# Kernel tuning notes

Hardware: AMD Instinct MI355X
Metric: run time of the kernel (lower is better)

Reference implementation:

```python
import jax, jax.numpy as jnp
import numpy as np

B, L, IN_DIM, D, H = 4, 1024, 256, 512, 8
DH = D // H
LARGE_NEG = -10000.0
LN_EPS = 1e-5


def _layernorm(x, g, b):
    mu = jnp.mean(x, axis=-1, keepdims=True)
    var = jnp.mean((x - mu) ** 2, axis=-1, keepdims=True)
    return (x - mu) * jax.lax.rsqrt(var + LN_EPS) * g + b


def setup_inputs() -> dict:
    key = jax.random.key(0)
    ks = jax.random.split(key, 16)
    s = 0.02
    return {
        "x": jax.random.normal(ks[0], (B, L, IN_DIM), jnp.float32),
        "attention_mask": jax.random.bernoulli(ks[1], 0.5, (B, L, L)),
        "adjacency_matrix": jax.random.uniform(ks[2], (B, L, L), jnp.float32),
        "W_fuse": jax.random.normal(ks[3], (D, IN_DIM), jnp.float32) * s,
        "b_fuse": jnp.zeros((D,), jnp.float32),
        "in_proj_w": jax.random.normal(ks[4], (3 * D, D), jnp.float32) * s,
        "in_proj_b": jnp.zeros((3 * D,), jnp.float32),
        "out_w": jax.random.normal(ks[5], (D, D), jnp.float32) * s,
        "out_b": jnp.zeros((D,), jnp.float32),
        "ln1_g": jnp.ones((D,), jnp.float32),
        "ln1_b": jnp.zeros((D,), jnp.float32),
        "ln2_g": jnp.ones((D,), jnp.float32),
        "ln2_b": jnp.zeros((D,), jnp.float32),
        "W1": jax.random.normal(ks[6], (4 * D, D), jnp.float32) * s,
        "b1": jnp.zeros((4 * D,), jnp.float32),
        "W2": jax.random.normal(ks[7], (D, 4 * D), jnp.float32) * s,
        "b2": jnp.zeros((D,), jnp.float32),
        "log_scale": jnp.array(0.0, jnp.float32),  # log(adj_bias_strength=1.0)
    }


def reference(x, attention_mask, adjacency_matrix, W_fuse, b_fuse, in_proj_w,
              in_proj_b, out_w, out_b, ln1_g, ln1_b, ln2_g, ln2_b,
              W1, b1, W2, b2, log_scale):
    # fuse projection (in_dim != d_model)
    x = jnp.einsum("bli,di->bld", x, W_fuse) + b_fuse

    # ensure_self_loops_in_mask: unmask diagonal of fully-masked rows
    eye = jnp.eye(L, dtype=bool)
    row_all = jnp.all(attention_mask, axis=-1)  # [B, L]
    mask = attention_mask & ~(eye[None, :, :] & row_all[:, :, None])

    # additive attention bias: large_neg where masked + scaled clipped adjacency
    bias = jnp.where(mask, LARGE_NEG, 0.0) + \
        jnp.exp(log_scale) * jnp.clip(adjacency_matrix, 0.0, 1.0)  # [B, L, L]

    # --- attention block (pre-norm) ---
    x_norm = _layernorm(x, ln1_g, ln1_b)
    qkv = jnp.einsum("bld,ed->ble", x_norm, in_proj_w) + in_proj_b
    q, k, v = jnp.split(qkv, 3, axis=-1)
    q = q.reshape(B, L, H, DH).transpose(0, 2, 1, 3)  # [B,H,L,DH]
    k = k.reshape(B, L, H, DH).transpose(0, 2, 1, 3)
    v = v.reshape(B, L, H, DH).transpose(0, 2, 1, 3)
    scores = jnp.einsum("bhqd,bhkd->bhqk", q, k) / np.sqrt(DH) + bias[:, None]
    probs = jax.nn.softmax(scores, axis=-1)
    ctx = jnp.einsum("bhqk,bhkd->bhqd", probs, v)
    ctx = ctx.transpose(0, 2, 1, 3).reshape(B, L, D)
    attn_out = jnp.einsum("bld,ed->ble", ctx, out_w) + out_b
    x = x + attn_out

    # --- FFN block (pre-norm) ---
    x_norm = _layernorm(x, ln2_g, ln2_b)
    h = jax.nn.gelu(jnp.einsum("bld,fd->blf", x_norm, W1) + b1, approximate=False)
    ff = jnp.einsum("blf,df->bld", h, W2) + b2
    return x + ff
```

## Files before the change

### kernel.cpp

```cpp
#include <hip/hip_runtime.h>
#include <math.h>

typedef unsigned short UST;
typedef __attribute__((ext_vector_type(8))) short bf16x8;
typedef __attribute__((ext_vector_type(4))) float f32x4;

#define BB 4
#define LL 1024
#define IND 256
#define DD 512
#define HH 8
#define FFD 2048
#define NT (BB*LL)

__device__ __forceinline__ float bf2f(UST u){ return __uint_as_float(((unsigned)u)<<16); }
__device__ __forceinline__ UST f2bf(float f){
  unsigned u = __float_as_uint(f);
  u += 0x7FFFu + ((u>>16)&1u);
  return (UST)(u>>16);
}
__device__ __forceinline__ float ldF(const void* p, long i, int isf32){
  return isf32 ? ((const float*)p)[i] : bf2f(((const UST*)p)[i]);
}
__device__ __forceinline__ bool ldMask(const void* p, long i, int fm){
  if (fm==0) return ((const int*)p)[i] != 0;
  if (fm==1) return ((const unsigned char*)p)[i] != 0;
  if (fm==2) return ((const UST*)p)[i] != 0;
  return ((const float*)p)[i] != 0.f;
}
__device__ __forceinline__ f32x4 mfma16(bf16x8 a, bf16x8 b, f32x4 c){
  return __builtin_amdgcn_mfma_f32_16x16x32_bf16(a, b, c, 0, 0, 0);
}
__device__ __forceinline__ void gld16(const void* g, void* l){
  __builtin_amdgcn_global_load_lds((const __attribute__((address_space(1))) unsigned int*)g,
                                   (__attribute__((address_space(3))) unsigned int*)l, 16, 0, 0);
}

__global__ void detect_k(int* flags, const UST* xh, const unsigned int* mw){
  int lane = threadIdx.x & 63;
  int e0 = (xh[lane] >> 7) & 0xFF;
  int e1 = (xh[64+lane] >> 7) & 0xFF;
  int f32 = __any((e0 >= 140) || (e1 >= 140)) ? 1 : 0;
  unsigned v = mw[lane];
  int w01   = __all(v <= 1u) ? 1 : 0;
  unsigned lo = v & 0xFFFFu, hi = v >> 16;
  int half  = __all((lo==0u||lo==0x3F80u) && (hi==0u||hi==0x3F80u)) ? 1 : 0;
  int wordF = __all(v==0u || v==0x3F800000u) ? 1 : 0;
  int byteB = __all((v & 0xFEFEFEFEu) == 0u) ? 1 : 0;
  if (lane == 0){
    flags[0] = f32;
    flags[1] = w01 ? 0 : (half ? (wordF ? 3 : 2) : (byteB ? 1 : 0));
  }
}

struct CvtArgs { const void* src[11]; UST* dst[11]; int n[11]; };
__global__ __launch_bounds__(256) void cvt_k(const int* flags, CvtArgs a){
  int ti = blockIdx.y;
  int n = a.n[ti];
  long i8 = ((long)blockIdx.x*256 + threadIdx.x)*8;
  if (i8 >= n) return;
  const void* s = a.src[ti]; UST* d = a.dst[ti];
  if (flags[0]){
    const float4* sf = (const float4*)s;
    float4 a0 = sf[i8>>2], a1 = sf[(i8>>2)+1];
    UST o[8] = { f2bf(a0.x),f2bf(a0.y),f2bf(a0.z),f2bf(a0.w),
                 f2bf(a1.x),f2bf(a1.y),f2bf(a1.z),f2bf(a1.w) };
    *(int4*)(d+i8) = *(const int4*)o;
  } else {
    ((int4*)d)[i8>>3] = ((const int4*)s)[i8>>3];
  }
}

__global__ __launch_bounds__(256) void bias_k(const int* flags, const void* mask,
                                              const void* adj, const void* lsp, UST* biasOut){
  int fF = flags[0], fM = flags[1];
  int row = blockIdx.x;
  int i = row & (LL-1);
  long base = (long)row * LL;
  int t = threadIdx.x;
  bool mv[4]; int my = 1;
  #pragma unroll
  for (int k = 0; k < 4; ++k){
    mv[k] = ldMask(mask, base + t + k*256, fM);
    my &= mv[k] ? 1 : 0;
  }
  int wa = __all(my);
  __shared__ int sAll[4];
  int w = t >> 6;
  if ((t & 63) == 0) sAll[w] = wa;
  __syncthreads();
  int rowAll = sAll[0] & sAll[1] & sAll[2] & sAll[3];
  float es = expf(ldF(lsp, 0, fF));
  #pragma unroll
  for (int k = 0; k < 4; ++k){
    int j = t + k*256;
    float a = ldF(adj, base + j, fF);
    a = fminf(fmaxf(a, 0.f), 1.f);
    bool eff = mv[k] && !((rowAll != 0) && (j == i));
    float bz = (eff ? -10000.f : 0.f) + es * a;
    biasOut[base + j] = f2bf(bz);
  }
}

template<int NI, int ACT, int RES, int OUTMODE>
__global__ __launch_bounds__(256) void gemm2_k(const int* flags,
    const UST* __restrict__ A, const UST* __restrict__ Bw, const UST* __restrict__ bias,
    const float* __restrict__ resid, void* Cout, int M, int N, int K){
  constexpr int TN = 32*NI;
  __shared__ UST sA[128*32];
  __shared__ UST sB[TN*32];
  int t = threadIdx.x, w = t>>6, lane = t&63, l15 = lane&15, qd = lane>>4;
  int m0 = blockIdx.x*128, n0 = blockIdx.y*TN;
  int wm = (w&1)*64, wn = (w>>1)*(NI*16);
  f32x4 acc[4][NI];
  #pragma unroll
  for (int mi=0; mi<4; ++mi)
    #pragma unroll
    for (int ni=0; ni<NI; ++ni){ acc[mi][ni][0]=0;acc[mi][ni][1]=0;acc[mi][ni][2]=0;acc[mi][ni][3]=0; }
  int arow = t>>2, acol = (t&3)*8;
  const UST* aSrc = A + (long)(m0+arow)*K + acol;
  const UST* bSrc = Bw + (long)(n0+arow)*K + acol;
  char* ldsA0 = (char*)sA + (w*64)*16;
  char* ldsA1 = (char*)sA + (256 + w*64)*16;
  char* ldsB0 = (char*)sB + (w*64)*16;
  char* ldsB1 = (char*)sB + (256 + w*64)*16;
  for (int k0 = 0; k0 < K; k0 += 32){
    __syncthreads();
    gld16(aSrc + k0, ldsA0);
    gld16(aSrc + 64*K + k0, ldsA1);
    gld16(bSrc + k0, ldsB0);
    if (NI == 4) gld16(bSrc + 64*K + k0, ldsB1);
    __syncthreads();
    bf16x8 afr[4], bfr[NI];
    #pragma unroll
    for (int mi=0; mi<4; ++mi) afr[mi] = *(const bf16x8*)&sA[(wm + mi*16 + l15)*32 + qd*8];
    #pragma unroll
    for (int ni=0; ni<NI; ++ni) bfr[ni] = *(const bf16x8*)&sB[(wn + ni*16 + l15)*32 + qd*8];
    #pragma unroll
    for (int mi=0; mi<4; ++mi)
      #pragma unroll
      for (int ni=0; ni<NI; ++ni)
        acc[mi][ni] = mfma16(afr[mi], bfr[ni], acc[mi][ni]);
  }
  int outF32 = (OUTMODE==1) || (OUTMODE==2 && flags[0]);
  #pragma unroll
  for (int mi=0; mi<4; ++mi){
    #pragma unroll
    for (int ni=0; ni<NI; ++ni){
      int gc = n0 + wn + ni*16 + l15;
      float bv = bf2f(bias[gc]);
      #pragma unroll
      for (int r=0; r<4; ++r){
        int grow = m0 + wm + mi*16 + qd*4 + r;
        float c = acc[mi][ni][r] + bv;
        if (ACT) c = 0.5f*c*(1.f+erff(c*0.70710678118654752f));
        long oi = (long)grow*N + gc;
        if (RES) c += resid[oi];
        if (outF32) ((float*)Cout)[oi] = c;
        else ((UST*)Cout)[oi] = f2bf(c);
      }
    }
  }
}

__global__ __launch_bounds__(256) void ln_k(const int* flags, const float* xin,
    const void* gp, const void* bp, UST* xout){
  int fF = flags[0];
  int row = blockIdx.x, t = threadIdx.x;
  const float* xr = xin + (long)row * DD;
  float v0 = xr[t], v1 = xr[t+256];
  float s = v0+v1, q = v0*v0 + v1*v1;
  #pragma unroll
  for (int off=1; off<64; off<<=1){ s += __shfl_xor(s,off,64); q += __shfl_xor(q,off,64); }
  __shared__ float rs[4], rq[4];
  int w = t>>6;
  if ((t&63)==0){ rs[w]=s; rq[w]=q; }
  __syncthreads();
  float S = rs[0]+rs[1]+rs[2]+rs[3];
  float Q = rq[0]+rq[1]+rq[2]+rq[3];
  float mean = S * (1.f/DD);
  float var  = fmaxf(Q * (1.f/DD) - mean*mean, 0.f);
  float ri = rsqrtf(var + 1e-5f);
  float g0 = ldF(gp, t, fF), b0 = ldF(bp, t, fF);
  float g1 = ldF(gp, t+256, fF), b1 = ldF(bp, t+256, fF);
  xout[(long)row*DD + t]     = f2bf((v0-mean)*ri*g0 + b0);
  xout[(long)row*DD + t+256] = f2bf((v1-mean)*ri*g1 + b1);
}

__global__ __launch_bounds__(256) void repack_v(const UST* __restrict__ qkv, UST* __restrict__ vT){
  int id = blockIdx.x;
  int bh = id & 31, qt = id >> 5;
  int b = bh >> 3, h = bh & 7;
  int t = threadIdx.x, w = t >> 6, lane = t & 63;
  int token = qt*64 + lane;
  const UST* src = qkv + ((long)(b*LL + token))*1536 + 1024 + h*64;
  #pragma unroll
  for (int c = 0; c < 2; ++c){
    int ch = w*2 + c;
    union { int4 v; UST u[8]; } uu;
    uu.v = *(const int4*)(src + ch*8);
    #pragma unroll
    for (int i = 0; i < 8; ++i)
      vT[((long)(bh*64 + ch*8 + i))*LL + token] = uu.u[i];
  }
}

__global__ __launch_bounds__(256) void attn_k(const UST* __restrict__ qkv,
    const UST* __restrict__ vT, const UST* __restrict__ bias, UST* __restrict__ ctx){
  int id = blockIdx.x;
  int b = id & 3, h = (id>>2) & 7, qt = id >> 5;
  int bh = b*HH + h;
  int q0 = qt*64;
  int t = threadIdx.x, w = t>>6, lane = t&63, l15 = lane&15, qd = lane>>4;
  __shared__ UST sP[4][16*80];
  UST* myP = &sP[w][0];
  const UST* qrow = qkv + ((long)(b*LL + q0 + w*16 + l15))*1536 + h*64;
  bf16x8 qf0 = *(const bf16x8*)(qrow + qd*8);
  bf16x8 qf1 = *(const bf16x8*)(qrow + 32 + qd*8);
  const UST* bptr[4];
  #pragma unroll
  for (int r=0;r<4;++r)
    bptr[r] = bias + ((long)b<<20) + (long)(q0 + w*16 + qd*4 + r)*LL + l15;
  const UST* kBase = qkv + (long)b*LL*1536 + 512 + h*64;
  const UST* vBase = vT + (long)bh*64*LL;
  f32x4 o[4]; float mr_[4], lr_[4];
  #pragma unroll
  for (int i=0;i<4;i++){ o[i][0]=0;o[i][1]=0;o[i][2]=0;o[i][3]=0; mr_[i]=-1e30f; lr_[i]=0.f; }
  const float LOG2E = 1.44269504f;
  for (int kt = 0; kt < 16; ++kt){
    int k0 = kt*64;
    f32x4 s4[4];
    #pragma unroll
    for (int i=0;i<4;i++){ s4[i][0]=0;s4[i][1]=0;s4[i][2]=0;s4[i][3]=0; }
    #pragma unroll
    for (int ni=0; ni<4; ++ni){
      const UST* kp = kBase + (long)(k0 + ni*16 + l15)*1536 + qd*8;
      bf16x8 kf0 = *(const bf16x8*)kp;
      bf16x8 kf1 = *(const bf16x8*)(kp + 32);
      s4[ni] = mfma16(qf0, kf0, s4[ni]);
      s4[ni] = mfma16(qf1, kf1, s4[ni]);
    }
    float sv[4][4];
    #pragma unroll
    for (int ni=0; ni<4; ++ni)
      #pragma unroll
      for (int r=0; r<4; ++r)
        sv[ni][r] = fmaf(s4[ni][r], 0.125f, bf2f(bptr[r][k0 + ni*16]));
    float alpha[4];
    #pragma unroll
    for (int r=0; r<4; ++r){
      float mcur = fmaxf(fmaxf(sv[0][r],sv[1][r]), fmaxf(sv[2][r],sv[3][r]));
      #pragma unroll
      for (int off=1; off<16; off<<=1) mcur = fmaxf(mcur, __shfl_xor(mcur,off,64));
      float mn = fmaxf(mr_[r], mcur);
      alpha[r] = exp2f((mr_[r]-mn)*LOG2E);
      mr_[r] = mn;
      float mn2 = mn*LOG2E;
      float psum = 0.f;
      #pragma unroll
      for (int ni=0; ni<4; ++ni){
        float p = exp2f(fmaf(sv[ni][r], LOG2E, -mn2));
        sv[ni][r] = p; psum += p;
      }
      #pragma unroll
      for (int off=1; off<16; off<<=1) psum += __shfl_xor(psum,off,64);
      lr_[r] = lr_[r]*alpha[r] + psum;
    }
    #pragma unroll
    for (int dn=0; dn<4; ++dn)
      #pragma unroll
      for (int r=0; r<4; ++r) o[dn][r] *= alpha[r];
    #pragma unroll
    for (int ni=0; ni<4; ++ni)
      #pragma unroll
      for (int r=0; r<4; ++r) myP[(qd*4+r)*80 + ni*16 + l15] = f2bf(sv[ni][r]);
    bf16x8 pf0 = *(const bf16x8*)&myP[l15*80 + qd*8];
    bf16x8 pf1 = *(const bf16x8*)&myP[l15*80 + 32 + qd*8];
    #pragma unroll
    for (int dn=0; dn<4; ++dn){
      const UST* vp = vBase + (long)(dn*16 + l15)*LL + k0 + qd*8;
      bf16x8 vf0 = *(const bf16x8*)vp;
      bf16x8 vf1 = *(const bf16x8*)(vp + 32);
      o[dn] = mfma16(pf0, vf0, o[dn]);
      o[dn] = mfma16(pf1, vf1, o[dn]);
    }
  }
  #pragma unroll
  for (int dn=0; dn<4; ++dn){
    #pragma unroll
    for (int r=0; r<4; ++r){
      long oi = ((long)(b*LL + q0 + w*16 + qd*4 + r))*DD + h*64 + dn*16 + l15;
      ctx[oi] = f2bf(o[dn][r] * (1.f/lr_[r]));
    }
  }
}

extern "C" void kernel_launch(void* const* d_in, const int* in_sizes, int n_in,
                              void* d_out, int out_size, void* d_ws, size_t ws_size,
                              hipStream_t stream){
  char* ws = (char*)d_ws;
  size_t o = 0;
  auto alloc = [&](size_t b){ size_t r = o; o += (b + 255) & ~(size_t)255; return r; };
  int*   flags = (int*)(ws + alloc(256));
  size_t biasOff = alloc(8UL<<20);
  size_t qkvOff  = alloc(12UL<<20);
  UST* biasC = (UST*)(ws + biasOff);
  UST* qkv   = (UST*)(ws + qkvOff);
  UST* hb    = (UST*)(ws + biasOff);
  UST* vT    = (UST*)(ws + alloc(4UL<<20));
  UST* xbf   = (UST*)(ws + alloc(2UL<<20));
  UST* wfuse = (UST*)(ws + alloc(131072*2));
  UST* bfuse = (UST*)(ws + alloc(1024));
  UST* ipw   = (UST*)(ws + alloc(786432*2));
  UST* ipb   = (UST*)(ws + alloc(3072*2));
  UST* outw  = (UST*)(ws + alloc(262144*2));
  UST* outb  = (UST*)(ws + alloc(1024));
  UST* w1    = (UST*)(ws + alloc(1048576*2));
  UST* b1    = (UST*)(ws + alloc(4096*2));
  UST* w2    = (UST*)(ws + alloc(1048576*2));
  UST* b2    = (UST*)(ws + alloc(1024));
  float* xf  = (float*)(ws + alloc((size_t)NT*DD*4));
  UST* xn    = (UST*)(ws + alloc((size_t)NT*DD*2));
  UST* ctx   = (UST*)(ws + alloc((size_t)NT*DD*2));
  float* x2  = (float*)(ws + alloc((size_t)NT*DD*4));

  detect_k<<<1, 64, 0, stream>>>(flags, (const UST*)d_in[0], (const unsigned int*)d_in[1]);

  CvtArgs ca;
  const int srcIdx[11] = {0,3,4,5,6,7,8,13,14,15,16};
  UST* dsts[11] = {xbf,wfuse,bfuse,ipw,ipb,outw,outb,w1,b1,w2,b2};
  const int ns[11] = {NT*IND, DD*IND, DD, 3*DD*DD, 3*DD, DD*DD, DD, FFD*DD, FFD, DD*FFD, DD};
  for (int i=0;i<11;i++){ ca.src[i]=d_in[srcIdx[i]]; ca.dst[i]=dsts[i]; ca.n[i]=ns[i]; }
  cvt_k<<<dim3(512,11), 256, 0, stream>>>(flags, ca);

  bias_k<<<BB*LL, 256, 0, stream>>>(flags, d_in[1], d_in[2], d_in[17], biasC);

  gemm2_k<2,0,0,1><<<dim3(32,8), 256, 0, stream>>>(flags, xbf, wfuse, bfuse, nullptr, xf, NT, DD, IND);
  ln_k<<<NT, 256, 0, stream>>>(flags, xf, d_in[9], d_in[10], xn);
  gemm2_k<4,0,0,0><<<dim3(32,12), 256, 0, stream>>>(flags, xn, ipw, ipb, nullptr, qkv, NT, 3*DD, DD);
  repack_v<<<512, 256, 0, stream>>>(qkv, vT);
  attn_k<<<512, 256, 0, stream>>>(qkv, vT, biasC, ctx);
  gemm2_k<2,0,1,1><<<dim3(32,8), 256, 0, stream>>>(flags, ctx, outw, outb, xf, x2, NT, DD, DD);
  ln_k<<<NT, 256, 0, stream>>>(flags, x2, d_in[11], d_in[12], xn);
  gemm2_k<4,1,0,0><<<dim3(32,16), 256, 0, stream>>>(flags, xn, w1, b1, nullptr, hb, NT, FFD, DD);
  gemm2_k<2,0,1,2><<<dim3(32,8), 256, 0, stream>>>(flags, hb, w2, b2, x2, d_out, NT, DD, FFD);
}
```

Before: 310.8 us.

## Stage K, V and bias tiles in shared memory for attention; vectorize bias kernel

The attention kernel now loads each 64-key tile of K, V^T and the bias block into LDS with 16-byte global-to-LDS loads (gld16) shared by all four waves, instead of each wave reading K, V and bias straight from global memory. The P scratch stride changes from 80 to 72. The bias kernel switches to contiguous 4-element-per-thread vectorized loads of mask and adjacency and a packed 8-byte store. The intent is to cut redundant global traffic and uncoalesced bias reads. The cost is two __syncthreads per tile with no double-buffering, and possible LDS bank conflicts in the 32-wide tiles.

Result: faster. 284.7 us (-8.4%).

```diff
diff --git a/kernel.cpp b/kernel.cpp
--- a/kernel.cpp
+++ b/kernel.cpp
@@ -78,12 +78,25 @@
   int i = row & (LL-1);
   long base = (long)row * LL;
   int t = threadIdx.x;
-  bool mv[4]; int my = 1;
-  #pragma unroll
-  for (int k = 0; k < 4; ++k){
-    mv[k] = ldMask(mask, base + t + k*256, fM);
-    my &= mv[k] ? 1 : 0;
-  }
+  int j0 = t*4;
+  bool mv[4];
+  if (fM == 0){
+    int4 m4 = *(const int4*)((const int*)mask + base + j0);
+    mv[0]=m4.x!=0; mv[1]=m4.y!=0; mv[2]=m4.z!=0; mv[3]=m4.w!=0;
+  } else {
+    #pragma unroll
+    for (int k=0;k<4;++k) mv[k] = ldMask(mask, base + j0 + k, fM);
+  }
+  float a4[4];
+  if (fF){
+    float4 av = *(const float4*)((const float*)adj + base + j0);
+    a4[0]=av.x; a4[1]=av.y; a4[2]=av.z; a4[3]=av.w;
+  } else {
+    const UST* ap = (const UST*)adj + base + j0;
+    #pragma unroll
+    for (int k=0;k<4;++k) a4[k] = bf2f(ap[k]);
+  }
+  int my = (mv[0]&&mv[1]&&mv[2]&&mv[3]) ? 1 : 0;
   int wa = __all(my);
   __shared__ int sAll[4];
   int w = t >> 6;
@@ -91,15 +104,15 @@
   __syncthreads();
   int rowAll = sAll[0] & sAll[1] & sAll[2] & sAll[3];
   float es = expf(ldF(lsp, 0, fF));
+  UST o4[4];
   #pragma unroll
   for (int k = 0; k < 4; ++k){
-    int j = t + k*256;
-    float a = ldF(adj, base + j, fF);
-    a = fminf(fmaxf(a, 0.f), 1.f);
+    int j = j0 + k;
+    float a = fminf(fmaxf(a4[k], 0.f), 1.f);
     bool eff = mv[k] && !((rowAll != 0) && (j == i));
-    float bz = (eff ? -10000.f : 0.f) + es * a;
-    biasOut[base + j] = f2bf(bz);
-  }
+    o4[k] = f2bf((eff ? -10000.f : 0.f) + es * a);
+  }
+  *(int2*)(biasOut + base + j0) = *(const int2*)o4;
 }
 
 template<int NI, int ACT, int RES, int OUTMODE>
@@ -212,40 +225,61 @@
   int bh = b*HH + h;
   int q0 = qt*64;
   int t = threadIdx.x, w = t>>6, lane = t&63, l15 = lane&15, qd = lane>>4;
-  __shared__ UST sP[4][16*80];
+  __shared__ UST sK0[64*32], sK1[64*32];
+  __shared__ UST sV0[64*32], sV1[64*32];
+  __shared__ UST sB0[64*32], sB1[64*32];
+  __shared__ UST sP[4][16*72];
   UST* myP = &sP[w][0];
+
   const UST* qrow = qkv + ((long)(b*LL + q0 + w*16 + l15))*1536 + h*64;
   bf16x8 qf0 = *(const bf16x8*)(qrow + qd*8);
   bf16x8 qf1 = *(const bf16x8*)(qrow + 32 + qd*8);
-  const UST* bptr[4];
-  #pragma unroll
-  for (int r=0;r<4;++r)
-    bptr[r] = bias + ((long)b<<20) + (long)(q0 + w*16 + qd*4 + r)*LL + l15;
-  const UST* kBase = qkv + (long)b*LL*1536 + 512 + h*64;
-  const UST* vBase = vT + (long)bh*64*LL;
+
+  int rowS = t>>2, colS = (t&3)*8;
+  const UST* kS = qkv + (long)(b*LL + rowS)*1536 + 512 + h*64 + colS;
+  const UST* vS = vT + (long)(bh*64 + rowS)*LL + colS;
+  const UST* bS = bias + ((long)b<<20) + (long)(q0 + rowS)*LL + colS;
+  char* dK0 = (char*)sK0 + w*1024; char* dK1 = (char*)sK1 + w*1024;
+  char* dV0 = (char*)sV0 + w*1024; char* dV1 = (char*)sV1 + w*1024;
+  char* dB0 = (char*)sB0 + w*1024; char* dB1 = (char*)sB1 + w*1024;
+
   f32x4 o[4]; float mr_[4], lr_[4];
   #pragma unroll
   for (int i=0;i<4;i++){ o[i][0]=0;o[i][1]=0;o[i][2]=0;o[i][3]=0; mr_[i]=-1e30f; lr_[i]=0.f; }
   const float LOG2E = 1.44269504f;
+
   for (int kt = 0; kt < 16; ++kt){
     int k0 = kt*64;
+    __syncthreads();
+    gld16(kS + (long)k0*1536,      dK0);
+    gld16(kS + (long)k0*1536 + 32, dK1);
+    gld16(vS + k0,                 dV0);
+    gld16(vS + k0 + 32,            dV1);
+    gld16(bS + k0,                 dB0);
+    gld16(bS + k0 + 32,            dB1);
+    __syncthreads();
+
     f32x4 s4[4];
     #pragma unroll
     for (int i=0;i<4;i++){ s4[i][0]=0;s4[i][1]=0;s4[i][2]=0;s4[i][3]=0; }
     #pragma unroll
     for (int ni=0; ni<4; ++ni){
-      const UST* kp = kBase + (long)(k0 + ni*16 + l15)*1536 + qd*8;
-      bf16x8 kf0 = *(const bf16x8*)kp;
-      bf16x8 kf1 = *(const bf16x8*)(kp + 32);
+      bf16x8 kf0 = *(const bf16x8*)&sK0[(ni*16+l15)*32 + qd*8];
+      bf16x8 kf1 = *(const bf16x8*)&sK1[(ni*16+l15)*32 + qd*8];
       s4[ni] = mfma16(qf0, kf0, s4[ni]);
       s4[ni] = mfma16(qf1, kf1, s4[ni]);
     }
     float sv[4][4];
     #pragma unroll
-    for (int ni=0; ni<4; ++ni)
-      #pragma unroll
-      for (int r=0; r<4; ++r)
-        sv[ni][r] = fmaf(s4[ni][r], 0.125f, bf2f(bptr[r][k0 + ni*16]));
+    for (int ni=0; ni<4; ++ni){
+      const UST* sBc = (ni < 2) ? sB0 : sB1;
+      int nc = (ni & 1)*16 + l15;
+      #pragma unroll
+      for (int r=0; r<4; ++r){
+        float bzv = bf2f(sBc[(w*16 + qd*4 + r)*32 + nc]);
+        sv[ni][r] = fmaf(s4[ni][r], 0.125f, bzv);
+      }
+    }
     float alpha[4];
     #pragma unroll
     for (int r=0; r<4; ++r){
@@ -273,14 +307,13 @@
     #pragma unroll
     for (int ni=0; ni<4; ++ni)
       #pragma unroll
-      for (int r=0; r<4; ++r) myP[(qd*4+r)*80 + ni*16 + l15] = f2bf(sv[ni][r]);
-    bf16x8 pf0 = *(const bf16x8*)&myP[l15*80 + qd*8];
-    bf16x8 pf1 = *(const bf16x8*)&myP[l15*80 + 32 + qd*8];
+      for (int r=0; r<4; ++r) myP[(qd*4+r)*72 + ni*16 + l15] = f2bf(sv[ni][r]);
+    bf16x8 pf0 = *(const bf16x8*)&myP[l15*72 + qd*8];
+    bf16x8 pf1 = *(const bf16x8*)&myP[l15*72 + 32 + qd*8];
     #pragma unroll
     for (int dn=0; dn<4; ++dn){
-      const UST* vp = vBase + (long)(dn*16 + l15)*LL + k0 + qd*8;
-      bf16x8 vf0 = *(const bf16x8*)vp;
-      bf16x8 vf1 = *(const bf16x8*)(vp + 32);
+      bf16x8 vf0 = *(const bf16x8*)&sV0[(dn*16+l15)*32 + qd*8];
+      bf16x8 vf1 = *(const bf16x8*)&sV1[(dn*16+l15)*32 + qd*8];
       o[dn] = mfma16(pf0, vf0, o[dn]);
       o[dn] = mfma16(pf1, vf1, o[dn]);
     }
```
